# Optimization experiments

Hardware: AMD Instinct MI355X
Metric: run time of the kernel (lower is better)

## Reference

```python
import jax, jax.numpy as jnp
import numpy as np

S = 14          # grid size
L_COORD = 5.0
L_NOOBJ = 0.5
BATCH = 4096


def setup_inputs() -> dict:
    key = jax.random.key(0)
    k1, k2, k3 = jax.random.split(key, 3)
    shape = (BATCH, S, S, 30)
    # strictly positive values so sqrt(w), sqrt(h) are well defined (as assumed by the torch code)
    pred = jax.random.uniform(k1, shape, dtype=jnp.float32, minval=0.01, maxval=1.0)
    target = jax.random.uniform(k2, shape, dtype=jnp.float32, minval=0.01, maxval=1.0)
    has_obj = (jax.random.uniform(k3, (BATCH, S, S)) < 0.3).astype(jnp.float32)
    target = target.at[..., 4].set(has_obj)
    return {"pred_tensor": pred, "target_tensor": target}


def _yolo_loss(pred_tensor, target_tensor):
    N = pred_tensor.shape[0]
    dt = pred_tensor.dtype

    obj = (target_tensor[..., 4] > 0).astype(dt)      # [N,S,S]
    noobj = (target_tensor[..., 4] == 0).astype(dt)   # [N,S,S]

    # ---- no-object confidence loss (channels 4 and 9 in cells without objects) ----
    d4 = pred_tensor[..., 4] - target_tensor[..., 4]
    d9 = pred_tensor[..., 9] - target_tensor[..., 9]
    no_object_loss = jnp.sum(noobj * (d4 * d4 + d9 * d9))

    # ---- class prediction loss (channels 10:30 in object cells) ----
    dcls = pred_tensor[..., 10:] - target_tensor[..., 10:]
    class_loss = jnp.sum(obj[..., None] * dcls * dcls)

    # ---- per-cell best-IoU box selection (vectorized over all cells) ----
    pboxes = pred_tensor[..., :10].reshape(N, S, S, 2, 5)    # [N,S,S,2,5]
    tboxes = target_tensor[..., :10].reshape(N, S, S, 2, 5)
    p = pboxes[..., :4]                                      # [N,S,S,2,4]
    t = tboxes[..., 0, :4]                                   # target box of the cell [N,S,S,4]

    # [x,y,w,h] (center+size, xy in grid units) -> corner coords
    p1 = p[..., :2] / S - p[..., 2:] / 2                     # [N,S,S,2,2]
    p2 = p[..., :2] / S + p[..., 2:] / 2
    t1 = t[..., :2] / S - t[..., 2:] / 2                     # [N,S,S,2]
    t2 = t[..., :2] / S + t[..., 2:] / 2

    lt = jnp.maximum(p1, t1[..., None, :])
    rb = jnp.minimum(p2, t2[..., None, :])
    wh = jnp.maximum(rb - lt, 0.0)
    inter = wh[..., 0] * wh[..., 1]                          # [N,S,S,2]
    area_p = (p2[..., 0] - p1[..., 0]) * (p2[..., 1] - p1[..., 1])
    area_t = ((t2[..., 0] - t1[..., 0]) * (t2[..., 1] - t1[..., 1]))[..., None]
    iou = inter / (area_p + area_t - inter)                  # [N,S,S,2]

    # torch code: if IoU[0] > IoU[1] pick box 0 else box 1 (ties -> box 1)
    pick1 = iou[..., 0] <= iou[..., 1]                       # [N,S,S] bool
    p_sel = jnp.where(pick1[..., None], pboxes[..., 1, :], pboxes[..., 0, :])  # [N,S,S,5]
    t_sel = jnp.where(pick1[..., None], tboxes[..., 1, :], tboxes[..., 0, :])
    iou_best = jnp.where(pick1, iou[..., 1], iou[..., 0])    # [N,S,S]

    dxy = p_sel[..., :2] - t_sel[..., :2]
    dwh = jnp.sqrt(p_sel[..., 2:4]) - jnp.sqrt(t_sel[..., 2:4])
    reg_loss = jnp.sum(obj[..., None] * dxy * dxy) + jnp.sum(obj[..., None] * dwh * dwh)

    # ---- containing-object confidence loss: pred conf vs best IoU ----
    dconf = p_sel[..., 4] - iou_best
    contain_loss = jnp.sum(obj * dconf * dconf)

    total = L_NOOBJ * no_object_loss + class_loss + L_COORD * reg_loss + contain_loss
    return total / N


def reference(pred_tensor, target_tensor):
    return _yolo_loss(pred_tensor, target_tensor)
```

## Files before the change

### kernel.cpp

```cpp
#include <hip/hip_runtime.h>

#define SDIM 14
#define L_COORD 5.0f
#define L_NOOBJ 0.5f
#define BATCH 4096
#define CELLS (BATCH * SDIM * SDIM)
#define BLOCK 256
#define NBLOCKS (CELLS / BLOCK)
#define CELL_F 30
#define BLK_F (BLOCK * CELL_F)
#define BLK_F4 (BLK_F / 4)

__global__ __launch_bounds__(BLOCK) void yolo_partial(
    const float* __restrict__ pred, const float* __restrict__ targ,
    float* __restrict__ partial) {
    __shared__ float s[2 * BLK_F];

    const size_t base = (size_t)blockIdx.x * BLK_F;
    const float4* pP = reinterpret_cast<const float4*>(pred + base);
    const float4* pT = reinterpret_cast<const float4*>(targ + base);
    float4* s4 = reinterpret_cast<float4*>(s);
#pragma unroll
    for (int j = 0; j < 15; ++j) {
        const int idx = threadIdx.x + j * BLOCK;
        const float4* src = (idx < BLK_F4) ? (pP + idx) : (pT + (idx - BLK_F4));
        s4[idx] = *src;
    }
    __syncthreads();

    const float* Pc = s + threadIdx.x * CELL_F;
    const float* Tc = s + BLK_F + threadIdx.x * CELL_F;

    float loss;
    if (Tc[4] > 0.0f) {
        float cls = 0.0f;
#pragma unroll
        for (int c = 10; c < 30; ++c) { float d = Pc[c] - Tc[c]; cls += d * d; }

        const float invS = 1.0f / (float)SDIM;
        const float t1x = Tc[0] * invS - Tc[2] * 0.5f;
        const float t1y = Tc[1] * invS - Tc[3] * 0.5f;
        const float t2x = Tc[0] * invS + Tc[2] * 0.5f;
        const float t2y = Tc[1] * invS + Tc[3] * 0.5f;
        const float area_t = (t2x - t1x) * (t2y - t1y);

        float iou0 = 0.0f, iou1 = 0.0f;
#pragma unroll
        for (int k = 0; k < 2; ++k) {
            const float bx = Pc[5 * k + 0], by = Pc[5 * k + 1];
            const float bw = Pc[5 * k + 2], bh = Pc[5 * k + 3];
            const float p1x = bx * invS - bw * 0.5f;
            const float p1y = by * invS - bh * 0.5f;
            const float p2x = bx * invS + bw * 0.5f;
            const float p2y = by * invS + bh * 0.5f;
            const float ltx = fmaxf(p1x, t1x), lty = fmaxf(p1y, t1y);
            const float rbx = fminf(p2x, t2x), rby = fminf(p2y, t2y);
            const float wx = fmaxf(rbx - ltx, 0.0f);
            const float wy = fmaxf(rby - lty, 0.0f);
            const float inter = wx * wy;
            const float area_p = (p2x - p1x) * (p2y - p1y);
            const float v = inter / (area_p + area_t - inter);
            if (k == 0) iou0 = v; else iou1 = v;
        }

        const bool pick1 = (iou0 <= iou1);
        const float iou_best = pick1 ? iou1 : iou0;
        const float psx = pick1 ? Pc[5] : Pc[0];
        const float psy = pick1 ? Pc[6] : Pc[1];
        const float psw = pick1 ? Pc[7] : Pc[2];
        const float psh = pick1 ? Pc[8] : Pc[3];
        const float psc = pick1 ? Pc[9] : Pc[4];
        const float tsx = pick1 ? Tc[5] : Tc[0];
        const float tsy = pick1 ? Tc[6] : Tc[1];
        const float tsw = pick1 ? Tc[7] : Tc[2];
        const float tsh = pick1 ? Tc[8] : Tc[3];

        const float dx = psx - tsx, dy = psy - tsy;
        const float dw = sqrtf(psw) - sqrtf(tsw);
        const float dh = sqrtf(psh) - sqrtf(tsh);
        const float reg = dx * dx + dy * dy + dw * dw + dh * dh;
        const float dconf = psc - iou_best;
        loss = cls + L_COORD * reg + dconf * dconf;
    } else {
        const float d4 = Pc[4] - Tc[4];
        const float d9 = Pc[9] - Tc[9];
        loss = L_NOOBJ * (d4 * d4 + d9 * d9);
    }

#pragma unroll
    for (int off = 32; off > 0; off >>= 1)
        loss += __shfl_down(loss, off, 64);

    __shared__ float wsum[BLOCK / 64];
    const int lane = threadIdx.x & 63;
    const int wave = threadIdx.x >> 6;
    if (lane == 0) wsum[wave] = loss;
    __syncthreads();
    if (threadIdx.x == 0)
        partial[blockIdx.x] = wsum[0] + wsum[1] + wsum[2] + wsum[3];
}

__global__ __launch_bounds__(BLOCK) void yolo_final(
    const float* __restrict__ partial, float* __restrict__ out) {
    float s = 0.0f;
    for (int i = threadIdx.x; i < NBLOCKS; i += BLOCK) s += partial[i];
#pragma unroll
    for (int off = 32; off > 0; off >>= 1)
        s += __shfl_down(s, off, 64);
    __shared__ float wsum[BLOCK / 64];
    const int lane = threadIdx.x & 63;
    const int wave = threadIdx.x >> 6;
    if (lane == 0) wsum[wave] = s;
    __syncthreads();
    if (threadIdx.x == 0)
        out[0] = (wsum[0] + wsum[1] + wsum[2] + wsum[3]) * (1.0f / (float)BATCH);
}

extern "C" void kernel_launch(void* const* d_in, const int* in_sizes, int n_in,
                              void* d_out, int out_size, void* d_ws, size_t ws_size,
                              hipStream_t stream) {
    const float* pred = (const float*)d_in[0];
    const float* targ = (const float*)d_in[1];
    float* out = (float*)d_out;
    float* partial = (float*)d_ws;

    yolo_partial<<<NBLOCKS, BLOCK, 0, stream>>>(pred, targ, partial);
    yolo_final<<<1, BLOCK, 0, stream>>>(partial, out);
}
```

Measured before the change: 205.7 us.

## Load cells directly from global memory and compute branch-free

Removes the shared-memory staging of each block's pred/target cells and has each thread read its own cell with float2 global loads. Both the object and no-object losses are computed unconditionally and selected at the end, avoiding wave divergence. This frees the large LDS allocation so more blocks can be resident, at the cost of strided, less coalesced per-thread loads that rely on caches.

```diff
diff --git a/kernel.cpp b/kernel.cpp
--- a/kernel.cpp
+++ b/kernel.cpp
@@ -8,84 +8,84 @@
 #define BLOCK 256
 #define NBLOCKS (CELLS / BLOCK)
 #define CELL_F 30
-#define BLK_F (BLOCK * CELL_F)
-#define BLK_F4 (BLK_F / 4)
 
-__global__ __launch_bounds__(BLOCK) void yolo_partial(
+__global__ __launch_bounds__(BLOCK, 4) void yolo_partial(
     const float* __restrict__ pred, const float* __restrict__ targ,
     float* __restrict__ partial) {
-    __shared__ float s[2 * BLK_F];
+    const int cell = blockIdx.x * BLOCK + threadIdx.x;
+    const float* P = pred + (size_t)cell * CELL_F;
+    const float* T = targ + (size_t)cell * CELL_F;
 
-    const size_t base = (size_t)blockIdx.x * BLK_F;
-    const float4* pP = reinterpret_cast<const float4*>(pred + base);
-    const float4* pT = reinterpret_cast<const float4*>(targ + base);
-    float4* s4 = reinterpret_cast<float4*>(s);
+    float Pb[10], Tb[10];
 #pragma unroll
-    for (int j = 0; j < 15; ++j) {
-        const int idx = threadIdx.x + j * BLOCK;
-        const float4* src = (idx < BLK_F4) ? (pP + idx) : (pT + (idx - BLK_F4));
-        s4[idx] = *src;
+    for (int j = 0; j < 5; ++j) {
+        const float2 a = *reinterpret_cast<const float2*>(P + 2 * j);
+        const float2 b = *reinterpret_cast<const float2*>(T + 2 * j);
+        Pb[2 * j] = a.x; Pb[2 * j + 1] = a.y;
+        Tb[2 * j] = b.x; Tb[2 * j + 1] = b.y;
     }
-    __syncthreads();
 
-    const float* Pc = s + threadIdx.x * CELL_F;
-    const float* Tc = s + BLK_F + threadIdx.x * CELL_F;
+    float cls = 0.0f;
+#pragma unroll
+    for (int j = 5; j < 15; ++j) {
+        const float2 a = *reinterpret_cast<const float2*>(P + 2 * j);
+        const float2 b = *reinterpret_cast<const float2*>(T + 2 * j);
+        const float dx = a.x - b.x;
+        const float dy = a.y - b.y;
+        cls += dx * dx;
+        cls += dy * dy;
+    }
 
-    float loss;
-    if (Tc[4] > 0.0f) {
-        float cls = 0.0f;
+    const float d4 = Pb[4] - Tb[4];
+    const float d9 = Pb[9] - Tb[9];
+    const float noobj_l = L_NOOBJ * (d4 * d4 + d9 * d9);
+
+    const float invS = 1.0f / (float)SDIM;
+    const float t1x = Tb[0] * invS - Tb[2] * 0.5f;
+    const float t1y = Tb[1] * invS - Tb[3] * 0.5f;
+    const float t2x = Tb[0] * invS + Tb[2] * 0.5f;
+    const float t2y = Tb[1] * invS + Tb[3] * 0.5f;
+    const float area_t = (t2x - t1x) * (t2y - t1y);
+
+    float iou0 = 0.0f, iou1 = 0.0f;
 #pragma unroll
-        for (int c = 10; c < 30; ++c) { float d = Pc[c] - Tc[c]; cls += d * d; }
+    for (int k = 0; k < 2; ++k) {
+        const float bx = Pb[5 * k + 0], by = Pb[5 * k + 1];
+        const float bw = Pb[5 * k + 2], bh = Pb[5 * k + 3];
+        const float p1x = bx * invS - bw * 0.5f;
+        const float p1y = by * invS - bh * 0.5f;
+        const float p2x = bx * invS + bw * 0.5f;
+        const float p2y = by * invS + bh * 0.5f;
+        const float ltx = fmaxf(p1x, t1x), lty = fmaxf(p1y, t1y);
+        const float rbx = fminf(p2x, t2x), rby = fminf(p2y, t2y);
+        const float wx = fmaxf(rbx - ltx, 0.0f);
+        const float wy = fmaxf(rby - lty, 0.0f);
+        const float inter = wx * wy;
+        const float area_p = (p2x - p1x) * (p2y - p1y);
+        const float v = inter / (area_p + area_t - inter);
+        if (k == 0) iou0 = v; else iou1 = v;
+    }
 
-        const float invS = 1.0f / (float)SDIM;
-        const float t1x = Tc[0] * invS - Tc[2] * 0.5f;
-        const float t1y = Tc[1] * invS - Tc[3] * 0.5f;
-        const float t2x = Tc[0] * invS + Tc[2] * 0.5f;
-        const float t2y = Tc[1] * invS + Tc[3] * 0.5f;
-        const float area_t = (t2x - t1x) * (t2y - t1y);
+    const bool pick1 = (iou0 <= iou1);
+    const float iou_best = pick1 ? iou1 : iou0;
+    const float psx = pick1 ? Pb[5] : Pb[0];
+    const float psy = pick1 ? Pb[6] : Pb[1];
+    const float psw = pick1 ? Pb[7] : Pb[2];
+    const float psh = pick1 ? Pb[8] : Pb[3];
+    const float psc = pick1 ? Pb[9] : Pb[4];
+    const float tsx = pick1 ? Tb[5] : Tb[0];
+    const float tsy = pick1 ? Tb[6] : Tb[1];
+    const float tsw = pick1 ? Tb[7] : Tb[2];
+    const float tsh = pick1 ? Tb[8] : Tb[3];
 
-        float iou0 = 0.0f, iou1 = 0.0f;
-#pragma unroll
-        for (int k = 0; k < 2; ++k) {
-            const float bx = Pc[5 * k + 0], by = Pc[5 * k + 1];
-            const float bw = Pc[5 * k + 2], bh = Pc[5 * k + 3];
-            const float p1x = bx * invS - bw * 0.5f;
-            const float p1y = by * invS - bh * 0.5f;
-            const float p2x = bx * invS + bw * 0.5f;
-            const float p2y = by * invS + bh * 0.5f;
-            const float ltx = fmaxf(p1x, t1x), lty = fmaxf(p1y, t1y);
-            const float rbx = fminf(p2x, t2x), rby = fminf(p2y, t2y);
-            const float wx = fmaxf(rbx - ltx, 0.0f);
-            const float wy = fmaxf(rby - lty, 0.0f);
-            const float inter = wx * wy;
-            const float area_p = (p2x - p1x) * (p2y - p1y);
-            const float v = inter / (area_p + area_t - inter);
-            if (k == 0) iou0 = v; else iou1 = v;
-        }
+    const float dx = psx - tsx, dy = psy - tsy;
+    const float dw = sqrtf(psw) - sqrtf(tsw);
+    const float dh = sqrtf(psh) - sqrtf(tsh);
+    const float reg = dx * dx + dy * dy + dw * dw + dh * dh;
+    const float dconf = psc - iou_best;
+    const float obj_l = cls + L_COORD * reg + dconf * dconf;
 
-        const bool pick1 = (iou0 <= iou1);
-        const float iou_best = pick1 ? iou1 : iou0;
-        const float psx = pick1 ? Pc[5] : Pc[0];
-        const float psy = pick1 ? Pc[6] : Pc[1];
-        const float psw = pick1 ? Pc[7] : Pc[2];
-        const float psh = pick1 ? Pc[8] : Pc[3];
-        const float psc = pick1 ? Pc[9] : Pc[4];
-        const float tsx = pick1 ? Tc[5] : Tc[0];
-        const float tsy = pick1 ? Tc[6] : Tc[1];
-        const float tsw = pick1 ? Tc[7] : Tc[2];
-        const float tsh = pick1 ? Tc[8] : Tc[3];
-
-        const float dx = psx - tsx, dy = psy - tsy;
-        const float dw = sqrtf(psw) - sqrtf(tsw);
-        const float dh = sqrtf(psh) - sqrtf(tsh);
-        const float reg = dx * dx + dy * dy + dw * dw + dh * dh;
-        const float dconf = psc - iou_best;
-        loss = cls + L_COORD * reg + dconf * dconf;
-    } else {
-        const float d4 = Pc[4] - Tc[4];
-        const float d9 = Pc[9] - Tc[9];
-        loss = L_NOOBJ * (d4 * d4 + d9 * d9);
-    }
+    float loss = (Tb[4] > 0.0f) ? obj_l : noobj_l;
 
 #pragma unroll
     for (int off = 32; off > 0; off >>= 1)
```

Measured after the change: 209.0 us. No clear change (+1.6%).
